# Kernel optimization log

Measured on AMD Instinct MI355X. Metric: run time of the kernel, lower is better.

Reference implementation:

```python
import jax, jax.numpy as jnp
import numpy as np

B, T, C, H = 2, 2048, 1024, 16  # batch, seq, n_embd, n_head


def setup_inputs() -> dict:
    key = jax.random.key(0)
    k1, k2, k3 = jax.random.split(key, 3)
    scale = 0.02
    return {
        "x": jax.random.normal(k1, (B, T, C), dtype=jnp.float32),
        "W_attn": jax.random.normal(k2, (3 * C, C), dtype=jnp.float32) * scale,
        "b_attn": jnp.zeros((3 * C,), dtype=jnp.float32),
        "W_proj": jax.random.normal(k3, (C, C), dtype=jnp.float32) * scale,
        "b_proj": jnp.zeros((C,), dtype=jnp.float32),
        "alpha": jnp.asarray(1.0, dtype=jnp.float32),
        "beta": jnp.asarray(0.1, dtype=jnp.float32),
        "gamma": jnp.asarray(0.1, dtype=jnp.float32),
    }


def reference(x, W_attn, b_attn, W_proj, b_proj, alpha, beta, gamma):
    Bx, Tx, Cx = x.shape
    d = Cx // H  # head dim
    qkv = x @ W_attn.T + b_attn                      # [B,T,3C]
    q, k, v = jnp.split(qkv, 3, axis=-1)

    def to_heads(t):
        return t.reshape(Bx, Tx, H, d).transpose(0, 2, 1, 3)  # [B,H,T,d]

    q, k, v = to_heads(q), to_heads(k), to_heads(v)

    inv_sqrt_d = jnp.asarray(1.0 / np.sqrt(d), dtype=x.dtype)
    scores = jnp.einsum('bhtd,bhsd->bhts', q, k) * inv_sqrt_d  # [B,H,T,T]

    causal = jnp.tril(jnp.ones((Tx, Tx), dtype=bool))
    scores = jnp.where(causal, scores, -jnp.inf)
    att = jax.nn.softmax(scores, axis=-1)

    # Id buffer = softmax(10000*eye) == identity; MC buffer = softmax(10000*tril)
    # == uniform causal prefix average: MC[i, j<=i] = 1/(i+1).
    id_m = jnp.eye(Tx, dtype=x.dtype)
    mc = causal.astype(x.dtype) / jnp.arange(1, Tx + 1, dtype=x.dtype)[:, None]

    shaped = beta * att + alpha * id_m - gamma * mc  # dropout p=0 -> identity
    y = jnp.einsum('bhts,bhsd->bhtd', shaped, v)     # [B,H,T,d]
    y = y.transpose(0, 2, 1, 3).reshape(Bx, Tx, Cx)
    return y @ W_proj.T + b_proj
```

## Files before the change

### kernel.cpp

```cpp
#include <hip/hip_runtime.h>
#include <stdint.h>

#define Bsz  2
#define Tseq 2048
#define Cemb 1024
#define NH   16
#define HD   64

typedef __attribute__((ext_vector_type(8))) __bf16 bf16x8;
typedef __attribute__((ext_vector_type(4))) float  f32x4;
typedef __attribute__((ext_vector_type(8))) unsigned short u16x8;

#define MFMA16(a, b, c) __builtin_amdgcn_mfma_f32_16x16x32_bf16((a), (b), (c), 0, 0, 0)

__device__ __forceinline__ unsigned short f2bf(float f) {
  union { float f; unsigned int u; } v; v.f = f;
  unsigned int u = v.u;
  u += 0x7fffu + ((u >> 16) & 1u);
  return (unsigned short)(u >> 16);
}
__device__ __forceinline__ float bf2f(unsigned short h) {
  union { unsigned int u; float f; } v; v.u = ((unsigned int)h) << 16;
  return v.f;
}
__device__ __forceinline__ unsigned int pack_bf2(float a, float b) {
  union { float f; unsigned int u; } va, vb; va.f = a; vb.f = b;
  return __builtin_amdgcn_perm(vb.u + 0x8000u, va.u + 0x8000u, 0x07060302u);
}

typedef __attribute__((address_space(1))) const unsigned int GU;
typedef __attribute__((address_space(3))) unsigned int LU;
__device__ __forceinline__ void load_lds16(const void* g, void* l) {
  __builtin_amdgcn_global_load_lds((GU*)g, (LU*)l, 16, 0, 0);
}

#define XE  4194304
#define WAE 3145728
__global__ void cast3_kernel(const float* __restrict__ x,
                             const float* __restrict__ wa,
                             const float* __restrict__ wp,
                             unsigned short* __restrict__ out) {
  const int i = (blockIdx.x * blockDim.x + threadIdx.x) * 4;
  const float* src;
  int off;
  if (i < XE) { src = x; off = i; }
  else if (i < XE + WAE) { src = wa; off = i - XE; }
  else { src = wp; off = i - (XE + WAE); }
  const float4 f = *(const float4*)(src + off);
  ushort4 o;
  o.x = f2bf(f.x); o.y = f2bf(f.y); o.z = f2bf(f.z); o.w = f2bf(f.w);
  *(ushort4*)(out + i) = o;
}

__global__ __launch_bounds__(256) void gemm_qkv_kernel(
    const unsigned short* __restrict__ A,
    const unsigned short* __restrict__ Bw,
    const float* __restrict__ bias,
    unsigned short* __restrict__ qkv) {
  const int K = Cemb;
  __shared__ unsigned short sA[128 * 64];
  __shared__ unsigned short sB[128 * 64];
  const int tid = threadIdx.x;
  const int wave = tid >> 6, lane = tid & 63;
  const int quad = lane >> 4, lrow = lane & 15;
  const int l7 = lrow & 7;
  const int wm = (wave >> 1) * 64, wn = (wave & 1) * 64;
  const int tileM = blockIdx.y * 128, tileN = blockIdx.x * 128;

  f32x4 acc[4][4];
#pragma unroll
  for (int i = 0; i < 4; ++i)
#pragma unroll
    for (int j = 0; j < 4; ++j) acc[i][j] = (f32x4){0.f, 0.f, 0.f, 0.f};

  for (int k0 = 0; k0 < K; k0 += 64) {
    __syncthreads();
#pragma unroll
    for (int s = 0; s < 4; ++s) {
      const int cid = tid + s * 256;
      const int r = cid >> 3, c = (cid & 7) ^ (r & 7);
      load_lds16(&A[(size_t)(tileM + r) * K + k0 + c * 8], &sA[cid * 8]);
      load_lds16(&Bw[(size_t)(tileN + r) * K + k0 + c * 8], &sB[cid * 8]);
    }
    __syncthreads();
#pragma unroll
    for (int half = 0; half < 2; ++half) {
      bf16x8 af[4], bfm[4];
#pragma unroll
      for (int mt = 0; mt < 4; ++mt)
        af[mt] = *(const bf16x8*)&sA[(wm + mt * 16 + lrow) * 64 +
                                     (((half * 4 + quad) ^ l7) << 3)];
#pragma unroll
      for (int nt = 0; nt < 4; ++nt)
        bfm[nt] = *(const bf16x8*)&sB[(wn + nt * 16 + lrow) * 64 +
                                      (((half * 4 + quad) ^ l7) << 3)];
#pragma unroll
      for (int mt = 0; mt < 4; ++mt)
#pragma unroll
        for (int nt = 0; nt < 4; ++nt)
          acc[mt][nt] = MFMA16(af[mt], bfm[nt], acc[mt][nt]);
    }
  }

  __syncthreads();
  unsigned short* sEp = sA + wave * 1024;
  float bias_v[4];
#pragma unroll
  for (int nt = 0; nt < 4; ++nt) bias_v[nt] = bias[tileN + wn + nt * 16 + lrow];
  const int gn0 = tileN + wn;
  const int part = gn0 >> 10, h = (gn0 & 1023) >> 6;

#pragma unroll
  for (int mt = 0; mt < 4; ++mt) {
#pragma unroll
    for (int nt = 0; nt < 4; ++nt)
#pragma unroll
      for (int reg = 0; reg < 4; ++reg) {
        const int q = quad * 4 + reg;
        const int ch = (nt * 2 + (lrow >> 3)) ^ (q & 7);
        sEp[q * 64 + ch * 8 + l7] = f2bf(acc[mt][nt][reg] + bias_v[nt]);
      }
    __builtin_amdgcn_wave_barrier();
#pragma unroll
    for (int i = 0; i < 2; ++i) {
      const int c = i * 64 + lane;
      const int r = c >> 3, ch2 = c & 7;
      const u16x8 row = *(const u16x8*)&sEp[r * 64 + ((ch2 ^ (r & 7)) << 3)];
      const int gm = tileM + wm + mt * 16 + r;
      const int bb = gm >> 11, t = gm & 2047;
      *(u16x8*)&qkv[((((size_t)part * Bsz + bb) * NH + h) * Tseq + t) * HD + ch2 * 8] = row;
    }
    __builtin_amdgcn_wave_barrier();
  }
}

__global__ __launch_bounds__(256) void gemm_proj_kernel(
    const unsigned short* __restrict__ A,
    const unsigned short* __restrict__ Bw,
    const float* __restrict__ bias,
    float* __restrict__ out) {
  const int K = Cemb;
  __shared__ unsigned short sA[128 * 64];
  __shared__ unsigned short sB[128 * 64];
  const int tid = threadIdx.x;
  const int wave = tid >> 6, lane = tid & 63;
  const int quad = lane >> 4, lrow = lane & 15;
  const int l7 = lrow & 7;
  const int wm = (wave >> 1) * 64, wn = (wave & 1) * 64;
  const int tileM = blockIdx.y * 128, tileN = blockIdx.x * 128;

  f32x4 acc[4][4];
#pragma unroll
  for (int i = 0; i < 4; ++i)
#pragma unroll
    for (int j = 0; j < 4; ++j) acc[i][j] = (f32x4){0.f, 0.f, 0.f, 0.f};

  for (int k0 = 0; k0 < K; k0 += 64) {
    __syncthreads();
#pragma unroll
    for (int s = 0; s < 4; ++s) {
      const int cid = tid + s * 256;
      const int r = cid >> 3, c = (cid & 7) ^ (r & 7);
      load_lds16(&A[(size_t)(tileM + r) * K + k0 + c * 8], &sA[cid * 8]);
      load_lds16(&Bw[(size_t)(tileN + r) * K + k0 + c * 8], &sB[cid * 8]);
    }
    __syncthreads();
#pragma unroll
    for (int half = 0; half < 2; ++half) {
      bf16x8 af[4], bfm[4];
#pragma unroll
      for (int mt = 0; mt < 4; ++mt)
        af[mt] = *(const bf16x8*)&sA[(wm + mt * 16 + lrow) * 64 +
                                     (((half * 4 + quad) ^ l7) << 3)];
#pragma unroll
      for (int nt = 0; nt < 4; ++nt)
        bfm[nt] = *(const bf16x8*)&sB[(wn + nt * 16 + lrow) * 64 +
                                      (((half * 4 + quad) ^ l7) << 3)];
#pragma unroll
      for (int mt = 0; mt < 4; ++mt)
#pragma unroll
        for (int nt = 0; nt < 4; ++nt)
          acc[mt][nt] = MFMA16(af[mt], bfm[nt], acc[mt][nt]);
    }
  }

#pragma unroll
  for (int mt = 0; mt < 4; ++mt)
#pragma unroll
    for (int nt = 0; nt < 4; ++nt)
#pragma unroll
      for (int reg = 0; reg < 4; ++reg) {
        const int gm = tileM + wm + mt * 16 + quad * 4 + reg;
        const int gn = tileN + wn + nt * 16 + lrow;
        out[(size_t)gm * Cemb + gn] = acc[mt][nt][reg] + bias[gn];
      }
}

__global__ __launch_bounds__(256) void attn_kernel(
    const unsigned short* __restrict__ qkv,
    const float* __restrict__ palpha, const float* __restrict__ pbeta,
    const float* __restrict__ pgamma,
    unsigned short* __restrict__ y) {
  __shared__ unsigned short sK[2][64 * 64];
  __shared__ unsigned short sVt[2][64 * 64];

  const int tid = threadIdx.x;
  const int wave = tid >> 6, lane = tid & 63;
  const int quad = lane >> 4, lrow = lane & 15;
  const int bh = blockIdx.y;
  const int b = bh >> 4, h = bh & 15;

  const size_t partStride = (size_t)Bsz * NH * Tseq * HD;
  const size_t headoff = (size_t)bh * Tseq * HD;
  const unsigned short* Q = qkv + headoff;
  const unsigned short* Kp = qkv + partStride + headoff;
  const unsigned short* Vp = qkv + 2 * partStride + headoff;

  const float alpha = palpha[0], beta = pbeta[0], gamma = pgamma[0];
  const float SCL = 0.125f * 1.44269504089f;

  union { unsigned short u[8]; bf16x8 v; } onesU;
#pragma unroll
  for (int j = 0; j < 8; ++j) onesU.u[j] = 0x3F80;
  const bf16x8 onesF = onesU.v;

  const int qtA = blockIdx.x;
  const int qtB = 31 - qtA;
  const int q0A = qtA * 64, q0B = qtB * 64;

  const int qrowA = q0A + wave * 16 + lrow;
  const int qrowB = q0B + wave * 16 + lrow;
  const bf16x8 bQA0 = *(const bf16x8*)&Q[(size_t)qrowA * HD + quad * 8];
  const bf16x8 bQA1 = *(const bf16x8*)&Q[(size_t)qrowA * HD + 32 + quad * 8];
  const bf16x8 bQB0 = *(const bf16x8*)&Q[(size_t)qrowB * HD + quad * 8];
  const bf16x8 bQB1 = *(const bf16x8*)&Q[(size_t)qrowB * HD + 32 + quad * 8];

  const int prow = ((lrow & 12) << 1) | (lrow & 3);

  f32x4 OtA[4], UtA[4], LA, OtB[4], UtB[4], LB;
#pragma unroll
  for (int dt = 0; dt < 4; ++dt) {
    OtA[dt] = (f32x4){0.f, 0.f, 0.f, 0.f};
    UtA[dt] = (f32x4){0.f, 0.f, 0.f, 0.f};
    OtB[dt] = (f32x4){0.f, 0.f, 0.f, 0.f};
    UtB[dt] = (f32x4){0.f, 0.f, 0.f, 0.f};
  }
  LA = (f32x4){0.f, 0.f, 0.f, 0.f};
  LB = (f32x4){0.f, 0.f, 0.f, 0.f};

  const int kr0 = tid >> 3, kc0 = tid & 7;
  const int hk = (kr0 & 7) ^ ((kr0 & 16) >> 2);
  const int vd0 = (tid & 31) * 2;
  const int vrb = (tid >> 5) * 8;
  const int vch = tid >> 5;
  const int hv0 = (vd0 & 7) ^ ((vd0 & 16) >> 2);
  const int hv1 = ((vd0 + 1) & 7) ^ (((vd0 + 1) & 16) >> 2);

  uint4 pk0, pk1;
  unsigned int pv[8];

  auto load_tile = [&](int it) {
    const int j0 = it * 64;
    pk0 = *(const uint4*)&Kp[(size_t)(j0 + kr0) * HD + kc0 * 8];
    pk1 = *(const uint4*)&Kp[(size_t)(j0 + 32 + kr0) * HD + kc0 * 8];
#pragma unroll
    for (int e = 0; e < 8; ++e)
      pv[e] = *(const unsigned int*)&Vp[(size_t)(j0 + vrb + e) * HD + vd0];
  };
  auto store_tile = [&](int buf) {
    unsigned short* K_ = sK[buf];
    unsigned short* Vt_ = sVt[buf];
    *(uint4*)&K_[kr0 * 64 + ((kc0 ^ hk) << 3)] = pk0;
    *(uint4*)&K_[(32 + kr0) * 64 + ((kc0 ^ hk) << 3)] = pk1;
    u16x8 lo, hi;
#pragma unroll
    for (int e = 0; e < 8; ++e) {
      lo[e] = (unsigned short)(pv[e] & 0xffffu);
      hi[e] = (unsigned short)(pv[e] >> 16);
    }
    *(u16x8*)&Vt_[vd0 * 64 + ((vch ^ hv0) << 3)] = lo;
    *(u16x8*)&Vt_[(vd0 + 1) * 64 + ((vch ^ hv1) << 3)] = hi;
  };

  load_tile(0);
  store_tile(0);

  const int ntiles = qtB + 1;
  for (int it = 0; it < ntiles; ++it) {
    const int cur = it & 1;
    __syncthreads();
    if (it + 1 < ntiles) load_tile(it + 1);

    const unsigned short* K_ = sK[cur];
    const unsigned short* Vt_ = sVt[cur];
    const int j0 = it * 64;
    const bool actA = (it <= qtA);
    const bool diagA = (it == qtA), diagB = (it == qtB);

    unsigned int pkA[4][2], pkB[4][2];
#pragma unroll
    for (int ct = 0; ct < 4; ++ct) {
      const int srow = (ct >> 1) * 32 + (ct & 1) * 4 + prow;
      const int hs = (srow & 7) ^ ((srow & 16) >> 2);
      const bf16x8 a0 = *(const bf16x8*)&K_[srow * 64 + ((quad ^ hs) << 3)];
      const bf16x8 a1 = *(const bf16x8*)&K_[srow * 64 + (((4 + quad) ^ hs) << 3)];
      const int sbase = j0 + (ct >> 1) * 32 + (ct & 1) * 4 + quad * 8;

      f32x4 sB = (f32x4){0.f, 0.f, 0.f, 0.f};
      sB = MFMA16(a0, bQB0, sB);
      sB = MFMA16(a1, bQB1, sB);
      float pB[4];
      if (diagB) {
#pragma unroll
        for (int reg = 0; reg < 4; ++reg)
          pB[reg] = exp2f((sbase + reg > qrowB) ? -1e30f : sB[reg] * SCL);
      } else {
#pragma unroll
        for (int reg = 0; reg < 4; ++reg) pB[reg] = exp2f(sB[reg] * SCL);
      }
      pkB[ct][0] = pack_bf2(pB[0], pB[1]);
      pkB[ct][1] = pack_bf2(pB[2], pB[3]);

      if (actA) {
        f32x4 sA = (f32x4){0.f, 0.f, 0.f, 0.f};
        sA = MFMA16(a0, bQA0, sA);
        sA = MFMA16(a1, bQA1, sA);
        float pA[4];
        if (diagA) {
#pragma unroll
          for (int reg = 0; reg < 4; ++reg)
            pA[reg] = exp2f((sbase + reg > qrowA) ? -1e30f : sA[reg] * SCL);
        } else {
#pragma unroll
          for (int reg = 0; reg < 4; ++reg) pA[reg] = exp2f(sA[reg] * SCL);
        }
        pkA[ct][0] = pack_bf2(pA[0], pA[1]);
        pkA[ct][1] = pack_bf2(pA[2], pA[3]);
      }
    }

    union { unsigned int w[4]; bf16x8 v; } tu;
    tu.w[0] = pkB[0][0]; tu.w[1] = pkB[0][1]; tu.w[2] = pkB[1][0]; tu.w[3] = pkB[1][1];
    const bf16x8 P1B = tu.v;
    tu.w[0] = pkB[2][0]; tu.w[1] = pkB[2][1]; tu.w[2] = pkB[3][0]; tu.w[3] = pkB[3][1];
    const bf16x8 P2B = tu.v;
    bf16x8 P1A = onesF, P2A = onesF;
    if (actA) {
      tu.w[0] = pkA[0][0]; tu.w[1] = pkA[0][1]; tu.w[2] = pkA[1][0]; tu.w[3] = pkA[1][1];
      P1A = tu.v;
      tu.w[0] = pkA[2][0]; tu.w[1] = pkA[2][1]; tu.w[2] = pkA[3][0]; tu.w[3] = pkA[3][1];
      P2A = tu.v;
    }

    LB = MFMA16(onesF, P1B, LB);
    LB = MFMA16(onesF, P2B, LB);
    if (actA) {
      LA = MFMA16(onesF, P1A, LA);
      LA = MFMA16(onesF, P2A, LA);
    }

    bf16x8 u1B = onesF, u2B = onesF, u1A = onesF, u2A = onesF;
    if (diagB) {
      union { unsigned short u[8]; bf16x8 v; } m0, m1;
#pragma unroll
      for (int jj = 0; jj < 8; ++jj) {
        m0.u[jj] = (j0 + quad * 8 + jj) <= qrowB ? (unsigned short)0x3F80 : (unsigned short)0;
        m1.u[jj] = (j0 + 32 + quad * 8 + jj) <= qrowB ? (unsigned short)0x3F80 : (unsigned short)0;
      }
      u1B = m0.v; u2B = m1.v;
    }
    if (actA && diagA) {
      union { unsigned short u[8]; bf16x8 v; } m0, m1;
#pragma unroll
      for (int jj = 0; jj < 8; ++jj) {
        m0.u[jj] = (j0 + quad * 8 + jj) <= qrowA ? (unsigned short)0x3F80 : (unsigned short)0;
        m1.u[jj] = (j0 + 32 + quad * 8 + jj) <= qrowA ? (unsigned short)0x3F80 : (unsigned short)0;
      }
      u1A = m0.v; u2A = m1.v;
    }

#pragma unroll
    for (int dt = 0; dt < 4; ++dt) {
      const int vr = dt * 16 + lrow;
      const int hvr = (vr & 7) ^ ((vr & 16) >> 2);
      const bf16x8 av0 = *(const bf16x8*)&Vt_[vr * 64 + ((quad ^ hvr) << 3)];
      const bf16x8 av1 = *(const bf16x8*)&Vt_[vr * 64 + (((4 + quad) ^ hvr) << 3)];
      OtB[dt] = MFMA16(av0, P1B, OtB[dt]);
      OtB[dt] = MFMA16(av1, P2B, OtB[dt]);
      UtB[dt] = MFMA16(av0, u1B, UtB[dt]);
      UtB[dt] = MFMA16(av1, u2B, UtB[dt]);
      if (actA) {
        OtA[dt] = MFMA16(av0, P1A, OtA[dt]);
        OtA[dt] = MFMA16(av1, P2A, OtA[dt]);
        UtA[dt] = MFMA16(av0, u1A, UtA[dt]);
        UtA[dt] = MFMA16(av1, u2A, UtA[dt]);
      }
    }

    if (it + 1 < ntiles) store_tile((it + 1) & 1);
  }

  auto epilogue = [&](const f32x4* Ot, const f32x4* Ut, const f32x4& L, int qrow) {
    const float bl = beta / L[0];
    const float gi = gamma / (float)(qrow + 1);
    const size_t ybase = ((size_t)b * Tseq + qrow) * Cemb + h * HD;
#pragma unroll
    for (int dt = 0; dt < 4; ++dt) {
      const int d0 = dt * 16 + quad * 4;
      const ushort4 vv4 = *(const ushort4*)&Vp[(size_t)qrow * HD + d0];
      const unsigned short vu[4] = {vv4.x, vv4.y, vv4.z, vv4.w};
      ushort4 o;
      unsigned short* op = (unsigned short*)&o;
#pragma unroll
      for (int reg = 0; reg < 4; ++reg) {
        const float yv = bl * Ot[dt][reg] + alpha * bf2f(vu[reg]) - gi * Ut[dt][reg];
        op[reg] = f2bf(yv);
      }
      *(ushort4*)&y[ybase + d0] = o;
    }
  };
  epilogue(OtA, UtA, LA, qrowA);
  epilogue(OtB, UtB, LB, qrowB);
}

extern "C" void kernel_launch(void* const* d_in, const int* in_sizes, int n_in,
                              void* d_out, int out_size, void* d_ws, size_t ws_size,
                              hipStream_t stream) {
  const float* x  = (const float*)d_in[0];
  const float* Wa = (const float*)d_in[1];
  const float* ba = (const float*)d_in[2];
  const float* Wp = (const float*)d_in[3];
  const float* bp = (const float*)d_in[4];
  const float* alpha = (const float*)d_in[5];
  const float* beta  = (const float*)d_in[6];
  const float* gamma = (const float*)d_in[7];
  float* out = (float*)d_out;

  unsigned short* ws = (unsigned short*)d_ws;
  unsigned short* xb   = ws;
  unsigned short* wab  = xb + (size_t)XE;
  unsigned short* wpb  = wab + (size_t)WAE;
  unsigned short* qkvb = wpb + (size_t)1024 * 1024;
  unsigned short* yb   = qkvb + (size_t)3 * Bsz * NH * Tseq * HD;

  cast3_kernel<<<(XE + WAE + 1048576) / 4 / 256, 256, 0, stream>>>(x, Wa, Wp, xb);

  gemm_qkv_kernel<<<dim3(3072 / 128, 4096 / 128), 256, 0, stream>>>(xb, wab, ba, qkvb);
  attn_kernel<<<dim3(16, Bsz * NH), 256, 0, stream>>>(qkvb, alpha, beta, gamma, yb);
  gemm_proj_kernel<<<dim3(1024 / 128, 4096 / 128), 256, 0, stream>>>(yb, wpb, bp, out);
}
```

Before: 213.3 us.

## Emit transposed V from QKV GEMM, async-stage attention tiles, retile GEMMs

The QKV GEMM epilogue now also writes a transposed V copy (per head, d-major over time) to a new workspace buffer. The attention kernel can then stage K and V^T tiles straight into LDS with async direct loads, replacing the old register-staged load and transposing store. Both GEMMs drop to a K-step of 32 with an unswizzled LDS layout, and the projection GEMM uses 64x128 tiles so it launches more blocks. This cuts register traffic and the in-kernel transpose, at the cost of extra global writes for V^T, more K-loop barriers, and possible LDS bank conflicts without the swizzle.

```diff
diff --git a/kernel.cpp b/kernel.cpp
--- a/kernel.cpp
+++ b/kernel.cpp
@@ -56,10 +56,11 @@
     const unsigned short* __restrict__ A,
     const unsigned short* __restrict__ Bw,
     const float* __restrict__ bias,
-    unsigned short* __restrict__ qkv) {
+    unsigned short* __restrict__ qkv,
+    unsigned short* __restrict__ vt) {
   const int K = Cemb;
-  __shared__ unsigned short sA[128 * 64];
-  __shared__ unsigned short sB[128 * 64];
+  __shared__ unsigned short sA[128 * 32];
+  __shared__ unsigned short sB[128 * 32];
   const int tid = threadIdx.x;
   const int wave = tid >> 6, lane = tid & 63;
   const int quad = lane >> 4, lrow = lane & 15;
@@ -73,33 +74,28 @@
 #pragma unroll
     for (int j = 0; j < 4; ++j) acc[i][j] = (f32x4){0.f, 0.f, 0.f, 0.f};
 
-  for (int k0 = 0; k0 < K; k0 += 64) {
+  for (int k0 = 0; k0 < K; k0 += 32) {
     __syncthreads();
 #pragma unroll
-    for (int s = 0; s < 4; ++s) {
+    for (int s = 0; s < 2; ++s) {
       const int cid = tid + s * 256;
-      const int r = cid >> 3, c = (cid & 7) ^ (r & 7);
-      load_lds16(&A[(size_t)(tileM + r) * K + k0 + c * 8], &sA[cid * 8]);
-      load_lds16(&Bw[(size_t)(tileN + r) * K + k0 + c * 8], &sB[cid * 8]);
+      const int r = cid >> 2, ko = (cid & 3) * 8;
+      load_lds16(&A[(size_t)(tileM + r) * K + k0 + ko], &sA[cid * 8]);
+      load_lds16(&Bw[(size_t)(tileN + r) * K + k0 + ko], &sB[cid * 8]);
     }
     __syncthreads();
-#pragma unroll
-    for (int half = 0; half < 2; ++half) {
-      bf16x8 af[4], bfm[4];
-#pragma unroll
-      for (int mt = 0; mt < 4; ++mt)
-        af[mt] = *(const bf16x8*)&sA[(wm + mt * 16 + lrow) * 64 +
-                                     (((half * 4 + quad) ^ l7) << 3)];
+    bf16x8 af[4], bfm[4];
+#pragma unroll
+    for (int mt = 0; mt < 4; ++mt)
+      af[mt] = *(const bf16x8*)&sA[(wm + mt * 16 + lrow) * 32 + quad * 8];
+#pragma unroll
+    for (int nt = 0; nt < 4; ++nt)
+      bfm[nt] = *(const bf16x8*)&sB[(wn + nt * 16 + lrow) * 32 + quad * 8];
+#pragma unroll
+    for (int mt = 0; mt < 4; ++mt)
 #pragma unroll
       for (int nt = 0; nt < 4; ++nt)
-        bfm[nt] = *(const bf16x8*)&sB[(wn + nt * 16 + lrow) * 64 +
-                                      (((half * 4 + quad) ^ l7) << 3)];
-#pragma unroll
-      for (int mt = 0; mt < 4; ++mt)
-#pragma unroll
-        for (int nt = 0; nt < 4; ++nt)
-          acc[mt][nt] = MFMA16(af[mt], bfm[nt], acc[mt][nt]);
-    }
+        acc[mt][nt] = MFMA16(af[mt], bfm[nt], acc[mt][nt]);
   }
 
   __syncthreads();
@@ -130,6 +126,22 @@
       const int bb = gm >> 11, t = gm & 2047;
       *(u16x8*)&qkv[((((size_t)part * Bsz + bb) * NH + h) * Tseq + t) * HD + ch2 * 8] = row;
     }
+    if (part == 2) {
+      unsigned int w[8];
+#pragma unroll
+      for (int q = 0; q < 16; q += 2) {
+        const unsigned short a0 =
+            sEp[q * 64 + (((lane >> 3) ^ (q & 7)) << 3) + (lane & 7)];
+        const unsigned short a1 =
+            sEp[(q + 1) * 64 + (((lane >> 3) ^ ((q + 1) & 7)) << 3) + (lane & 7)];
+        w[q >> 1] = (unsigned int)a0 | ((unsigned int)a1 << 16);
+      }
+      const int gm0 = tileM + wm + mt * 16;
+      const int bb = gm0 >> 11, t0 = gm0 & 2047;
+      unsigned short* dst = &vt[(((size_t)bb * NH + h) * HD + lane) * Tseq + t0];
+      *(uint4*)(dst) = *(const uint4*)&w[0];
+      *(uint4*)(dst + 8) = *(const uint4*)&w[4];
+    }
     __builtin_amdgcn_wave_barrier();
   }
 }
@@ -140,57 +152,54 @@
     const float* __restrict__ bias,
     float* __restrict__ out) {
   const int K = Cemb;
-  __shared__ unsigned short sA[128 * 64];
-  __shared__ unsigned short sB[128 * 64];
+  __shared__ unsigned short sA[64 * 32];
+  __shared__ unsigned short sB[128 * 32];
   const int tid = threadIdx.x;
   const int wave = tid >> 6, lane = tid & 63;
   const int quad = lane >> 4, lrow = lane & 15;
-  const int l7 = lrow & 7;
-  const int wm = (wave >> 1) * 64, wn = (wave & 1) * 64;
-  const int tileM = blockIdx.y * 128, tileN = blockIdx.x * 128;
-
-  f32x4 acc[4][4];
+  const int wn = wave * 32;
+  const int tileM = blockIdx.y * 64, tileN = blockIdx.x * 128;
+
+  f32x4 acc[4][2];
 #pragma unroll
   for (int i = 0; i < 4; ++i)
 #pragma unroll
-    for (int j = 0; j < 4; ++j) acc[i][j] = (f32x4){0.f, 0.f, 0.f, 0.f};
-
-  for (int k0 = 0; k0 < K; k0 += 64) {
+    for (int j = 0; j < 2; ++j) acc[i][j] = (f32x4){0.f, 0.f, 0.f, 0.f};
+
+  for (int k0 = 0; k0 < K; k0 += 32) {
     __syncthreads();
-#pragma unroll
-    for (int s = 0; s < 4; ++s) {
-      const int cid = tid + s * 256;
-      const int r = cid >> 3, c = (cid & 7) ^ (r & 7);
-      load_lds16(&A[(size_t)(tileM + r) * K + k0 + c * 8], &sA[cid * 8]);
-      load_lds16(&Bw[(size_t)(tileN + r) * K + k0 + c * 8], &sB[cid * 8]);
+    {
+      const int rA = tid >> 2, koA = (tid & 3) * 8;
+      load_lds16(&A[(size_t)(tileM + rA) * K + k0 + koA], &sA[tid * 8]);
+#pragma unroll
+      for (int s = 0; s < 2; ++s) {
+        const int cB = tid + s * 256;
+        const int rB = cB >> 2, koB = (cB & 3) * 8;
+        load_lds16(&Bw[(size_t)(tileN + rB) * K + k0 + koB], &sB[cB * 8]);
+      }
     }
     __syncthreads();
-#pragma unroll
-    for (int half = 0; half < 2; ++half) {
-      bf16x8 af[4], bfm[4];
-#pragma unroll
-      for (int mt = 0; mt < 4; ++mt)
-        af[mt] = *(const bf16x8*)&sA[(wm + mt * 16 + lrow) * 64 +
-                                     (((half * 4 + quad) ^ l7) << 3)];
-#pragma unroll
-      for (int nt = 0; nt < 4; ++nt)
-        bfm[nt] = *(const bf16x8*)&sB[(wn + nt * 16 + lrow) * 64 +
-                                      (((half * 4 + quad) ^ l7) << 3)];
-#pragma unroll
-      for (int mt = 0; mt < 4; ++mt)
-#pragma unroll
-        for (int nt = 0; nt < 4; ++nt)
-          acc[mt][nt] = MFMA16(af[mt], bfm[nt], acc[mt][nt]);
-    }
+    bf16x8 af[4], bfm[2];
+#pragma unroll
+    for (int mt = 0; mt < 4; ++mt)
+      af[mt] = *(const bf16x8*)&sA[(mt * 16 + lrow) * 32 + quad * 8];
+#pragma unroll
+    for (int nt = 0; nt < 2; ++nt)
+      bfm[nt] = *(const bf16x8*)&sB[(wn + nt * 16 + lrow) * 32 + quad * 8];
+#pragma unroll
+    for (int mt = 0; mt < 4; ++mt)
+#pragma unroll
+      for (int nt = 0; nt < 2; ++nt)
+        acc[mt][nt] = MFMA16(af[mt], bfm[nt], acc[mt][nt]);
   }
 
 #pragma unroll
   for (int mt = 0; mt < 4; ++mt)
 #pragma unroll
-    for (int nt = 0; nt < 4; ++nt)
+    for (int nt = 0; nt < 2; ++nt)
 #pragma unroll
       for (int reg = 0; reg < 4; ++reg) {
-        const int gm = tileM + wm + mt * 16 + quad * 4 + reg;
+        const int gm = tileM + mt * 16 + quad * 4 + reg;
         const int gn = tileN + wn + nt * 16 + lrow;
         out[(size_t)gm * Cemb + gn] = acc[mt][nt][reg] + bias[gn];
       }
@@ -198,6 +207,7 @@
 
 __global__ __launch_bounds__(256) void attn_kernel(
     const unsigned short* __restrict__ qkv,
+    const unsigned short* __restrict__ vt,
     const float* __restrict__ palpha, const float* __restrict__ pbeta,
     const float* __restrict__ pgamma,
     unsigned short* __restrict__ y) {
@@ -215,6 +225,7 @@
   const unsigned short* Q = qkv + headoff;
   const unsigned short* Kp = qkv + partStride + headoff;
   const unsigned short* Vp = qkv + 2 * partStride + headoff;
+  const unsigned short* Vt_g = vt + (size_t)bh * HD * Tseq;
 
   const float alpha = palpha[0], beta = pbeta[0], gamma = pgamma[0];
   const float SCL = 0.125f * 1.44269504089f;
@@ -248,48 +259,25 @@
   LA = (f32x4){0.f, 0.f, 0.f, 0.f};
   LB = (f32x4){0.f, 0.f, 0.f, 0.f};
 
-  const int kr0 = tid >> 3, kc0 = tid & 7;
-  const int hk = (kr0 & 7) ^ ((kr0 & 16) >> 2);
-  const int vd0 = (tid & 31) * 2;
-  const int vrb = (tid >> 5) * 8;
-  const int vch = tid >> 5;
-  const int hv0 = (vd0 & 7) ^ ((vd0 & 16) >> 2);
-  const int hv1 = ((vd0 + 1) & 7) ^ (((vd0 + 1) & 16) >> 2);
-
-  uint4 pk0, pk1;
-  unsigned int pv[8];
-
-  auto load_tile = [&](int it) {
+  auto stage_tile = [&](int it, int buf) {
     const int j0 = it * 64;
-    pk0 = *(const uint4*)&Kp[(size_t)(j0 + kr0) * HD + kc0 * 8];
-    pk1 = *(const uint4*)&Kp[(size_t)(j0 + 32 + kr0) * HD + kc0 * 8];
-#pragma unroll
-    for (int e = 0; e < 8; ++e)
-      pv[e] = *(const unsigned int*)&Vp[(size_t)(j0 + vrb + e) * HD + vd0];
+#pragma unroll
+    for (int s = 0; s < 2; ++s) {
+      const int c = tid + s * 256;
+      const int r = c >> 3, cc = c & 7;
+      const int pk = cc ^ (r & 7) ^ ((r & 16) >> 2);
+      load_lds16(&Kp[(size_t)(j0 + r) * HD + pk * 8], &sK[buf][c * 8]);
+      load_lds16(&Vt_g[(size_t)r * Tseq + j0 + pk * 8], &sVt[buf][c * 8]);
+    }
   };
-  auto store_tile = [&](int buf) {
-    unsigned short* K_ = sK[buf];
-    unsigned short* Vt_ = sVt[buf];
-    *(uint4*)&K_[kr0 * 64 + ((kc0 ^ hk) << 3)] = pk0;
-    *(uint4*)&K_[(32 + kr0) * 64 + ((kc0 ^ hk) << 3)] = pk1;
-    u16x8 lo, hi;
-#pragma unroll
-    for (int e = 0; e < 8; ++e) {
-      lo[e] = (unsigned short)(pv[e] & 0xffffu);
-      hi[e] = (unsigned short)(pv[e] >> 16);
-    }
-    *(u16x8*)&Vt_[vd0 * 64 + ((vch ^ hv0) << 3)] = lo;
-    *(u16x8*)&Vt_[(vd0 + 1) * 64 + ((vch ^ hv1) << 3)] = hi;
-  };
-
-  load_tile(0);
-  store_tile(0);
+
+  stage_tile(0, 0);
 
   const int ntiles = qtB + 1;
   for (int it = 0; it < ntiles; ++it) {
     const int cur = it & 1;
     __syncthreads();
-    if (it + 1 < ntiles) load_tile(it + 1);
+    if (it + 1 < ntiles) stage_tile(it + 1, (it + 1) & 1);
 
     const unsigned short* K_ = sK[cur];
     const unsigned short* Vt_ = sVt[cur];
@@ -396,8 +384,6 @@
         UtA[dt] = MFMA16(av1, u2A, UtA[dt]);
       }
     }
-
-    if (it + 1 < ntiles) store_tile((it + 1) & 1);
   }
 
   auto epilogue = [&](const f32x4* Ot, const f32x4* Ut, const f32x4& L, int qrow) {
@@ -442,10 +428,11 @@
   unsigned short* wpb  = wab + (size_t)WAE;
   unsigned short* qkvb = wpb + (size_t)1024 * 1024;
   unsigned short* yb   = qkvb + (size_t)3 * Bsz * NH * Tseq * HD;
+  unsigned short* vtb  = yb + (size_t)Bsz * Tseq * Cemb;
 
   cast3_kernel<<<(XE + WAE + 1048576) / 4 / 256, 256, 0, stream>>>(x, Wa, Wp, xb);
 
-  gemm_qkv_kernel<<<dim3(3072 / 128, 4096 / 128), 256, 0, stream>>>(xb, wab, ba, qkvb);
-  attn_kernel<<<dim3(16, Bsz * NH), 256, 0, stream>>>(qkvb, alpha, beta, gamma, yb);
-  gemm_proj_kernel<<<dim3(1024 / 128, 4096 / 128), 256, 0, stream>>>(yb, wpb, bp, out);
-}
+  gemm_qkv_kernel<<<dim3(3072 / 128, 4096 / 128), 256, 0, stream>>>(xb, wab, ba, qkvb, vtb);
+  attn_kernel<<<dim3(16, Bsz * NH), 256, 0, stream>>>(qkvb, vtb, alpha, beta, gamma, yb);
+  gemm_proj_kernel<<<dim3(1024 / 128, 4096 / 64), 256, 0, stream>>>(yb, wpb, bp, out);
+}
```

Result: faster. 199.7 us (-6.4%).
